# Optimization experiments

Hardware: AMD Instinct MI355X
Metric: run time of the kernel (lower is better)

Reference implementation:

```python
import jax, jax.numpy as jnp
import numpy as np

B, C, H, W = 4, 64, 256, 256
DS = 4        # ClusterLocalAtt downscale
CS = 2        # FastClusterAtt cluster_stride
NH = 4        # FastClusterAtt num_heads
G = 4         # OrthoConvClustering groups
N_NOISE = 8   # number of -1 (noise) labels; even and divisible by B


def _maxpool(x, k):
    b, c, h, w = x.shape
    return x.reshape(b, c, h // k, k, w // k, k).max(axis=(3, 5))


def _normalize(x, eps=1e-12):
    n = jnp.linalg.norm(x, axis=-1, keepdims=True)
    return x / jnp.maximum(n, eps)


def _feat_sim(cf, nf):
    # cf: (B,k,HW), nf: (B,n,HW) -> (B,k) mean cosine similarity over noise rows
    return jnp.einsum('bkl,bnl->bkn', _normalize(cf), _normalize(nf)).mean(-1)


def setup_inputs():
    key = jax.random.key(0)
    ks = jax.random.split(key, 12)
    x = jax.random.normal(ks[0], (B, C, H, W), jnp.float32)
    noise_idx = jnp.arange(N_NOISE, dtype=jnp.int32)
    labels = jax.random.randint(ks[1], (B * C,), 0, 12, dtype=jnp.int32)
    labels = labels.at[noise_idx].set(-1)
    inv = 1.0 / np.sqrt(C // G)
    return {
        'x': x, 'labels': labels, 'noise_idx': noise_idx,
        'qkv_w1': jax.random.normal(ks[2], (3 * C,), jnp.float32) * 0.5,
        'qkv_b1': jax.random.normal(ks[3], (3 * C,), jnp.float32) * 0.1,
        'up_k': jax.random.normal(ks[4], (C, DS, DS), jnp.float32) * 0.25,
        'up_b': jax.random.normal(ks[5], (C,), jnp.float32) * 0.1,
        'clu_w': jax.random.normal(ks[6], (G, C // G, C // G), jnp.float32) * inv,
        'clu_b': jnp.zeros((C,), jnp.float32),
        'qkv_w2': jax.random.normal(ks[7], (3 * C,), jnp.float32) * 0.5,
        'bais_w': jax.random.normal(ks[8], (C, C), jnp.float32) * (inv * 0.5),
        'bais_b': jax.random.normal(ks[9], (C,), jnp.float32) * 0.1,
    }


def reference(x, labels, noise_idx, qkv_w1, qkv_b1, up_k, up_b,
              clu_w, clu_b, qkv_w2, bais_w, bais_b):
    idx3 = jnp.arange(3 * C) // 3  # grouped 1x1 conv (groups=C): out ch j reads in ch j//3
    # ================= ClusterLocalAtt =================
    x_down = _maxpool(x, DS)                        # (B,C,Hd,Wd)
    Hd, Wd = H // DS, W // DS
    hw = Hd * Wd
    qkv = x_down[:, idx3] * qkv_w1[None, :, None, None] + qkv_b1[None, :, None, None]
    qkv = qkv.reshape(3 * B * C, hw)                # torch: reshape(1, 3*B*C, hw)
    q, k, v = jnp.split(qkv, 3, axis=0)             # each (B*C, hw) - batch/ch mixed, faithful
    valid = labels != -1
    allowed = (labels[:, None] == labels[None, :]) & valid[:, None] & valid[None, :]
    scores = q @ k.T                                # (BC, BC)
    attn = jax.nn.softmax(jnp.where(allowed, scores, -1e30), axis=-1)
    att = jnp.where(valid[:, None], attn @ v, 0.0)  # noise rows stay zero
    out = att.reshape(B, C, Hd, Wd)
    # depthwise ConvTranspose2d(kernel=DS, stride=DS): each input px -> DSxDS block
    up = jnp.einsum('bchw,cpq->bchpwq', out, up_k).reshape(B, C, H, W)
    up = up + up_b[None, :, None, None]
    noise = x.reshape(B * C, H * W)[noise_idx].reshape(B, N_NOISE // B, H * W)
    sim = _feat_sim(up.reshape(B, C, H * W), noise)[:, :, None, None]  # (B,C,1,1)
    out_clu = x + (up + (1.0 - sim) * x)
    # ================= FastClusterAtt =================
    xf = out_clu.reshape(B, G, C // G, H * W)
    xc = jnp.einsum('goi,bgil->bgol', clu_w, xf).reshape(B, C, H * W) + clu_b[None, :, None]
    x_ds = _maxpool(xc.reshape(B, C, H, W), CS)     # (B,C,Hs,Ws)
    Hs, Ws = H // CS, W // CS
    Ls = Hs * Ws
    qkv2 = (x_ds[:, idx3] * qkv_w2[None, :, None, None]).reshape(B, 3, NH, C // NH, Ls)
    qh, kh, vh = qkv2[:, 0], qkv2[:, 1], qkv2[:, 2]  # (B,NH,hd,Ls)
    sc = (qh * kh).sum(axis=2, keepdims=True) / np.sqrt(C // NH)  # (B,NH,1,Ls)
    a = jax.nn.softmax(sc, axis=-1)
    oh = (a * vh).sum(axis=-1).reshape(B, C)        # (B,C) global pooled heads
    # bilinear upsample of a spatially-constant map is the same constant -> skip interp
    ov = jnp.einsum('oc,bc->bo', bais_w, oh) + bais_b
    out_full = jnp.broadcast_to(ov[:, :, None, None], (B, C, H, W))
    sim2 = _feat_sim(out_full.reshape(B, C, H * W), noise)[:, :, None, None]
    WWT = jnp.einsum('goi,gpi->gop', clu_w, clu_w)
    I = jnp.eye(C // G, dtype=clu_w.dtype)
    ortho = 1.0 - jax.lax.stop_gradient(jnp.mean((WWT - I) ** 2))
    out2 = out_full * (1.0 - sim2) + ortho * out_clu
    return out_clu + out2
```

## Files before the change

kernel.cpp:

```cpp
#include <hip/hip_runtime.h>
#include <math.h>

#define WS_XD     0u
#define WS_S      1048576u
#define WS_GPART  1048832u
#define WS_G      2097408u
#define WS_COEF   2113792u
#define WS_CONST  2138368u
#define WS_ATT    2138624u
#define WS_FAC    3187200u
#define WS_XDS    3187456u
#define WS_OH     7381760u
#define WS_ALPHA  7382016u
#define WS_BETA   7382272u
#define WS_NSTAT  7382273u
#define WS_P2     7382304u

__device__ __forceinline__ float bsum(float v, float* sd, int tid) {
    sd[tid] = v; __syncthreads();
    for (int off = 128; off > 0; off >>= 1) {
        if (tid < off) sd[tid] += sd[tid + off];
        __syncthreads();
    }
    float r = sd[0]; __syncthreads(); return r;
}
__device__ __forceinline__ float bmax(float v, float* sd, int tid) {
    sd[tid] = v; __syncthreads();
    for (int off = 128; off > 0; off >>= 1) {
        if (tid < off) sd[tid] = fmaxf(sd[tid], sd[tid + off]);
        __syncthreads();
    }
    float r = sd[0]; __syncthreads(); return r;
}

__global__ __launch_bounds__(256) void k_noise(const float* __restrict__ x,
                                               const int* __restrict__ nidx,
                                               float* __restrict__ ws) {
    __shared__ float sd[256];
    int n = blockIdx.x, tid = threadIdx.x;
    const float4* xr = (const float4*)x + (size_t)nidx[n] * 16384;
    float s = 0.f, ss = 0.f;
    for (int it = 0; it < 64; ++it) {
        float4 v = xr[it * 256 + tid];
        s  += v.x + v.y + v.z + v.w;
        ss += v.x*v.x + v.y*v.y + v.z*v.z + v.w*v.w;
    }
    float st = bsum(s, sd, tid);
    float sst = bsum(ss, sd, tid);
    if (tid == 0) { ws[WS_NSTAT + n] = st; ws[WS_NSTAT + 8 + n] = sqrtf(sst); }
}

__global__ __launch_bounds__(256) void k_pool4(const float* __restrict__ x,
                                               float* __restrict__ ws) {
    __shared__ float sd[256];
    int r = blockIdx.x, tid = threadIdx.x;
    const float4* xr = (const float4*)x + (size_t)r * 16384;
    float* xd = ws + WS_XD + (size_t)r * 4096;
    float sum = 0.f;
    for (int it = 0; it < 16; ++it) {
        int o = it * 256 + tid;
        int h = o >> 6, w = o & 63;
        float m = -INFINITY;
        #pragma unroll
        for (int p = 0; p < 4; ++p) {
            float4 v = xr[(4 * h + p) * 64 + w];
            m = fmaxf(m, fmaxf(fmaxf(v.x, v.y), fmaxf(v.z, v.w)));
        }
        xd[o] = m; sum += m;
    }
    float st = bsum(sum, sd, tid);
    if (tid == 0) ws[WS_S + r] = st;
}

__global__ __launch_bounds__(256) void k_gram(float* __restrict__ ws) {
    __shared__ __align__(16) float As[64][68];
    __shared__ __align__(16) float Bs[64][68];
    int tid = threadIdx.x, tx = tid & 15, ty = tid >> 4;
    int ra0 = blockIdx.y * 64, rb0 = 80 + blockIdx.x * 64, k0 = blockIdx.z * 64;
    const float4* xd4 = (const float4*)(ws + WS_XD);
    #pragma unroll
    for (int q = 0; q < 4; ++q) {
        int idx = q * 256 + tid;
        int row = idx >> 4, cf = idx & 15;
        float4 a = xd4[(size_t)(ra0 + row) * 1024 + (k0 >> 2) + cf];
        As[cf*4+0][row] = a.x; As[cf*4+1][row] = a.y; As[cf*4+2][row] = a.z; As[cf*4+3][row] = a.w;
        float4 b = xd4[(size_t)(rb0 + row) * 1024 + (k0 >> 2) + cf];
        Bs[cf*4+0][row] = b.x; Bs[cf*4+1][row] = b.y; Bs[cf*4+2][row] = b.z; Bs[cf*4+3][row] = b.w;
    }
    __syncthreads();
    float acc[4][4] = {};
    #pragma unroll 4
    for (int kk = 0; kk < 64; ++kk) {
        float4 a = *(const float4*)&As[kk][ty * 4];
        float4 b = *(const float4*)&Bs[kk][tx * 4];
        acc[0][0] += a.x*b.x; acc[0][1] += a.x*b.y; acc[0][2] += a.x*b.z; acc[0][3] += a.x*b.w;
        acc[1][0] += a.y*b.x; acc[1][1] += a.y*b.y; acc[1][2] += a.y*b.z; acc[1][3] += a.y*b.w;
        acc[2][0] += a.z*b.x; acc[2][1] += a.z*b.y; acc[2][2] += a.z*b.z; acc[2][3] += a.z*b.w;
        acc[3][0] += a.w*b.x; acc[3][1] += a.w*b.y; acc[3][2] += a.w*b.z; acc[3][3] += a.w*b.w;
    }
    float* gp = ws + WS_GPART + (size_t)blockIdx.z * 16384;
    #pragma unroll
    for (int i = 0; i < 4; ++i) {
        float4 o = make_float4(acc[i][0], acc[i][1], acc[i][2], acc[i][3]);
        *(float4*)&gp[(size_t)(ra0 + ty * 4 + i) * 128 + blockIdx.x * 64 + tx * 4] = o;
    }
}

__global__ __launch_bounds__(256) void k_gred(float* __restrict__ ws) {
    int t = blockIdx.x * 256 + threadIdx.x;
    const float4* gp = (const float4*)(ws + WS_GPART);
    float4 s = make_float4(0.f, 0.f, 0.f, 0.f);
    for (int p = 0; p < 64; ++p) {
        float4 v = gp[(size_t)p * 4096 + t];
        s.x += v.x; s.y += v.y; s.z += v.z; s.w += v.w;
    }
    ((float4*)(ws + WS_G))[t] = s;
}

__global__ __launch_bounds__(256) void k_attn1(const int* __restrict__ labels,
                                               const float* __restrict__ w1,
                                               const float* __restrict__ b1,
                                               float* __restrict__ ws) {
    __shared__ float sd[256];
    __shared__ float attn_s[256];
    int i = blockIdx.x, tid = threadIdx.x;
    int labi = labels[i];
    bool validi = (labi != -1);
    int bi = (i >= 192) ? 1 : 0;
    int ji = i - bi * 192;
    int rq = bi * 64 + ji / 3;
    float wq = w1[ji], bq = b1[ji];
    int gk = 256 + tid;
    int bk = (gk >= 384) ? 2 : 1;
    int jk = gk - bk * 192;
    int rk = bk * 64 + jk / 3;
    float wk = w1[jk], bbk = b1[jk];
    int labj = labels[tid];
    bool allowed = validi && (labj == labi) && (labj != -1);
    float score = wq * wk * ws[WS_G + rq * 128 + (rk - 80)]
                + wq * bbk * ws[WS_S + rq]
                + wk * bq  * ws[WS_S + rk]
                + 4096.0f * bq * bbk;
    float sc = allowed ? score : -1e30f;
    float m = bmax(sc, sd, tid);
    float e = __expf(sc - m);
    float Z = bsum(e, sd, tid);
    float attn = validi ? (e / Z) : 0.0f;
    attn_s[tid] = attn;
    int gv = 512 + tid;
    int bv = (gv >= 576) ? 3 : 2;
    int jv = gv - bv * 192;
    float csum = bsum(attn * b1[jv], sd, tid);
    if (tid < 96) {
        float s = 0.0f;
        if (tid < 86) {
            int rv = 170 + tid;
            int lo, hi, jadd;
            if (rv < 192) { int c = rv - 128; lo = 3 * c; if (lo < 128) lo = 128; hi = 3 * c + 2; jadd = -128; }
            else          { int c = rv - 192; lo = 3 * c; hi = 3 * c + 2; jadd = 64; }
            for (int jj = lo; jj <= hi; ++jj) s += attn_s[jj + jadd] * w1[jj];
        }
        ws[WS_COEF + i * 96 + tid] = s;
    }
    if (tid == 0) ws[WS_CONST + i] = csum;
}

__global__ __launch_bounds__(256) void k_attmm(float* __restrict__ ws) {
    __shared__ __align__(16) float As[96][68];
    __shared__ __align__(16) float Bs[96][64];
    int tid = threadIdx.x, tx = tid & 15, ty = tid >> 4;
    int col0 = blockIdx.x * 64, row0 = blockIdx.y * 64;
    const float4* cf4 = (const float4*)(ws + WS_COEF);
    const float4* xd4 = (const float4*)(ws + WS_XD);
    #pragma unroll
    for (int q = 0; q < 6; ++q) {
        int f = q * 256 + tid;
        {
            int row = f / 24, c24 = f - row * 24;
            float4 v = cf4[(size_t)(row0 + row) * 24 + c24];
            As[c24*4+0][row] = v.x; As[c24*4+1][row] = v.y; As[c24*4+2][row] = v.z; As[c24*4+3][row] = v.w;
        }
        {
            int row = f >> 4, c16 = f & 15;
            float4 v = make_float4(0.f, 0.f, 0.f, 0.f);
            if (row < 86) v = xd4[(size_t)(170 + row) * 1024 + (col0 >> 2) + c16];
            *(float4*)&Bs[row][c16 * 4] = v;
        }
    }
    __syncthreads();
    float acc[4][4] = {};
    #pragma unroll 4
    for (int kk = 0; kk < 96; ++kk) {
        float4 a = *(const float4*)&As[kk][ty * 4];
        float4 b = *(const float4*)&Bs[kk][tx * 4];
        acc[0][0] += a.x*b.x; acc[0][1] += a.x*b.y; acc[0][2] += a.x*b.z; acc[0][3] += a.x*b.w;
        acc[1][0] += a.y*b.x; acc[1][1] += a.y*b.y; acc[1][2] += a.y*b.z; acc[1][3] += a.y*b.w;
        acc[2][0] += a.z*b.x; acc[2][1] += a.z*b.y; acc[2][2] += a.z*b.z; acc[2][3] += a.z*b.w;
        acc[3][0] += a.w*b.x; acc[3][1] += a.w*b.y; acc[3][2] += a.w*b.z; acc[3][3] += a.w*b.w;
    }
    float* att = ws + WS_ATT;
    #pragma unroll
    for (int i = 0; i < 4; ++i) {
        int row = row0 + ty * 4 + i;
        float cv = ws[WS_CONST + row];
        float4 o = make_float4(acc[i][0] + cv, acc[i][1] + cv, acc[i][2] + cv, acc[i][3] + cv);
        *(float4*)&att[(size_t)row * 4096 + col0 + tx * 4] = o;
    }
}

__global__ __launch_bounds__(256) void k_sim(const float* __restrict__ x,
                                             const int* __restrict__ nidx,
                                             const float* __restrict__ upk,
                                             const float* __restrict__ upb,
                                             float* __restrict__ ws) {
    __shared__ float sd[256];
    int r = blockIdx.x, tid = threadIdx.x;
    int b = r >> 6, c = r & 63;
    const float* att = ws + WS_ATT + (size_t)r * 4096;
    const float4* xn0 = (const float4*)x + (size_t)nidx[2 * b] * 16384;
    const float4* xn1 = (const float4*)x + (size_t)nidx[2 * b + 1] * 16384;
    const float4* k4p = (const float4*)upk + c * 4;
    float ub = upb[c];
    float4 kk0 = k4p[0], kk1 = k4p[1], kk2 = k4p[2], kk3 = k4p[3];
    float s2 = 0.f, d0 = 0.f, d1 = 0.f;
    for (int it = 0; it < 64; ++it) {
        int f = it * 256 + tid;
        int rowf = f >> 6, c4 = f & 63;
        float av = att[(rowf >> 2) * 64 + c4];
        int p = rowf & 3;
        float4 kv = (p == 0) ? kk0 : ((p == 1) ? kk1 : ((p == 2) ? kk2 : kk3));
        float4 a0 = xn0[f], a1 = xn1[f];
        float u;
        u = av * kv.x + ub; s2 += u * u; d0 += u * a0.x; d1 += u * a1.x;
        u = av * kv.y + ub; s2 += u * u; d0 += u * a0.y; d1 += u * a1.y;
        u = av * kv.z + ub; s2 += u * u; d0 += u * a0.z; d1 += u * a1.z;
        u = av * kv.w + ub; s2 += u * u; d0 += u * a0.w; d1 += u * a1.w;
    }
    s2 = bsum(s2, sd, tid);
    d0 = bsum(d0, sd, tid);
    d1 = bsum(d1, sd, tid);
    if (tid == 0) {
        float nup = fmaxf(sqrtf(s2), 1e-12f);
        float n0 = fmaxf(ws[WS_NSTAT + 8 + 2 * b], 1e-12f);
        float n1 = fmaxf(ws[WS_NSTAT + 8 + 2 * b + 1], 1e-12f);
        float sim = 0.5f * (d0 / (nup * n0) + d1 / (nup * n1));
        ws[WS_FAC + r] = 2.0f - sim;
    }
}

__global__ __launch_bounds__(256) void k_cluds(const float* __restrict__ x,
                                               const float* __restrict__ upk,
                                               const float* __restrict__ upb,
                                               const float* __restrict__ cw,
                                               const float* __restrict__ cb,
                                               float* __restrict__ ws) {
    __shared__ float wcl[256];
    __shared__ float kup[256];
    __shared__ float cbl[16], ubl[16], fcl[16];
    int h2 = blockIdx.x, g = blockIdx.y, b = blockIdx.z;
    int t = threadIdx.x;
    wcl[t] = cw[g * 256 + t];
    kup[t] = upk[g * 256 + t];
    if (t < 16) {
        cbl[t] = cb[g * 16 + t];
        ubl[t] = upb[g * 16 + t];
        fcl[t] = ws[WS_FAC + b * 64 + g * 16 + t];
    }
    __syncthreads();
    int r0 = 2 * h2;
    int h_att = h2 >> 1, p0 = r0 & 3;
    int wa = t >> 2, q = t & 3;
    float oc0[16], oc1[16];
    const float* attb = ws + WS_ATT;
    #pragma unroll
    for (int i = 0; i < 16; ++i) {
        int cch = g * 16 + i;
        float av = attb[(size_t)(b * 64 + cch) * 4096 + h_att * 64 + wa];
        float u0 = av * kup[i * 16 + p0 * 4 + q] + ubl[i];
        float u1 = av * kup[i * 16 + (p0 + 1) * 4 + q] + ubl[i];
        const float* xrow = x + (size_t)(b * 64 + cch) * 65536;
        float x0 = xrow[r0 * 256 + t];
        float x1 = xrow[(r0 + 1) * 256 + t];
        oc0[i] = u0 + fcl[i] * x0;
        oc1[i] = u1 + fcl[i] * x1;
    }
    float* xds = ws + WS_XDS;
    #pragma unroll
    for (int o = 0; o < 16; ++o) {
        float a0 = cbl[o], a1 = cbl[o];
        #pragma unroll
        for (int i = 0; i < 16; ++i) {
            a0 += wcl[o * 16 + i] * oc0[i];
            a1 += wcl[o * 16 + i] * oc1[i];
        }
        float m = fmaxf(a0, a1);
        m = fmaxf(m, __shfl_xor(m, 1));
        if ((t & 1) == 0)
            xds[(size_t)((b * 64 + g * 16 + o) * 128 + h2) * 128 + (t >> 1)] = m;
    }
}

__global__ __launch_bounds__(256) void k_attn2a(const float* __restrict__ w2,
                                                float* __restrict__ ws) {
    __shared__ float ms[256], dsh[256];
    __shared__ float ns[256][16];
    int chunk = blockIdx.x, nh = blockIdx.y, b = blockIdx.z, tid = threadIdx.x;
    const float* X = ws + WS_XDS + (size_t)b * 1048576;
    float wqd[16], wkd[16], wvd[16];
    int oq[16], ok[16], ovo[16];
    #pragma unroll
    for (int d = 0; d < 16; ++d) {
        int jq = nh * 16 + d, jk = 64 + nh * 16 + d, jv = 128 + nh * 16 + d;
        wqd[d] = w2[jq]; wkd[d] = w2[jk]; wvd[d] = w2[jv];
        oq[d] = (jq / 3) * 16384; ok[d] = (jk / 3) * 16384; ovo[d] = (jv / 3) * 16384;
    }
    float m = -INFINITY, den = 0.f, num[16];
    #pragma unroll
    for (int d = 0; d < 16; ++d) num[d] = 0.f;
    #pragma unroll
    for (int e = 0; e < 2; ++e) {
        int l = chunk * 512 + e * 256 + tid;
        float sc = 0.f;
        #pragma unroll
        for (int d = 0; d < 16; ++d) sc += (X[oq[d] + l] * wqd[d]) * (X[ok[d] + l] * wkd[d]);
        sc *= 0.25f;
        float nm = fmaxf(m, sc);
        float rr = __expf(m - nm), ee = __expf(sc - nm);
        den = den * rr + ee;
        #pragma unroll
        for (int d = 0; d < 16; ++d) num[d] = num[d] * rr + ee * (X[ovo[d] + l] * wvd[d]);
        m = nm;
    }
    ms[tid] = m; dsh[tid] = den;
    #pragma unroll
    for (int d = 0; d < 16; ++d) ns[tid][d] = num[d];
    __syncthreads();
    for (int off = 128; off > 0; off >>= 1) {
        if (tid < off) {
            float ma = ms[tid], mb = ms[tid + off];
            float M = fmaxf(ma, mb);
            float ra = __expf(ma - M), rb = __expf(mb - M);
            dsh[tid] = dsh[tid] * ra + dsh[tid + off] * rb;
            #pragma unroll
            for (int d = 0; d < 16; ++d)
                ns[tid][d] = ns[tid][d] * ra + ns[tid + off][d] * rb;
            ms[tid] = M;
        }
        __syncthreads();
    }
    if (tid == 0) {
        float* p = ws + WS_P2 + ((size_t)(b * 4 + nh) * 32 + chunk) * 18;
        p[0] = ms[0]; p[1] = dsh[0];
        #pragma unroll
        for (int d = 0; d < 16; ++d) p[2 + d] = ns[0][d];
    }
}

__global__ __launch_bounds__(64) void k_attn2b(float* __restrict__ ws) {
    int bh = blockIdx.x;
    int lane = threadIdx.x;
    float m = -INFINITY, den = 0.f, num[16];
    #pragma unroll
    for (int d = 0; d < 16; ++d) num[d] = 0.f;
    if (lane < 32) {
        const float* p = ws + WS_P2 + ((size_t)bh * 32 + lane) * 18;
        m = p[0]; den = p[1];
        #pragma unroll
        for (int d = 0; d < 16; ++d) num[d] = p[2 + d];
    }
    #pragma unroll
    for (int mask = 1; mask <= 16; mask <<= 1) {
        float mo = __shfl_xor(m, mask);
        float dn = __shfl_xor(den, mask);
        float M = fmaxf(m, mo);
        float ra = __expf(m - M), rb = __expf(mo - M);
        den = den * ra + dn * rb;
        #pragma unroll
        for (int d = 0; d < 16; ++d) {
            float no = __shfl_xor(num[d], mask);
            num[d] = num[d] * ra + no * rb;
        }
        m = M;
    }
    __shared__ float outn[16];
    __shared__ float outd;
    if (lane == 0) {
        outd = den;
        #pragma unroll
        for (int d = 0; d < 16; ++d) outn[d] = num[d];
    }
    __syncthreads();
    if (lane < 16) {
        int b = bh >> 2, nh = bh & 3;
        ws[WS_OH + b * 64 + nh * 16 + lane] = outn[lane] / outd;
    }
}

__global__ __launch_bounds__(256) void k_head(const float* __restrict__ bw,
                                              const float* __restrict__ bb,
                                              const float* __restrict__ cw,
                                              float* __restrict__ ws) {
    __shared__ float ohs[256], sd[256];
    int tid = threadIdx.x;
    ohs[tid] = ws[WS_OH + tid];
    __syncthreads();
    int b = tid >> 6, o = tid & 63;
    float s = bb[o];
    #pragma unroll 4
    for (int c2 = 0; c2 < 64; ++c2) s += bw[o * 64 + c2] * ohs[b * 64 + c2];
    float oacc = 0.f;
    for (int u = 0; u < 4; ++u) {
        int e = tid * 4 + u;
        int g = e >> 8, oo = (e >> 4) & 15, p = e & 15;
        float ss = 0.f;
        #pragma unroll
        for (int i = 0; i < 16; ++i) ss += cw[g * 256 + oo * 16 + i] * cw[g * 256 + p * 16 + i];
        float dd = ss - ((oo == p) ? 1.0f : 0.0f);
        oacc += dd * dd;
    }
    float tot = bsum(oacc, sd, tid);
    float nd = fmaxf(fabsf(s) * 256.0f, 1e-12f);
    float t0 = ws[WS_NSTAT + 2 * b], t1 = ws[WS_NSTAT + 2 * b + 1];
    float n0 = fmaxf(ws[WS_NSTAT + 8 + 2 * b], 1e-12f);
    float n1 = fmaxf(ws[WS_NSTAT + 8 + 2 * b + 1], 1e-12f);
    float sim2 = (s / nd) * 0.5f * (t0 / n0 + t1 / n1);
    ws[WS_ALPHA + tid] = (1.0f - sim2) * s;
    if (tid == 0) ws[WS_BETA] = 2.0f - tot / 1024.0f;
}

__global__ __launch_bounds__(256) void k_final(const float* __restrict__ x,
                                               const float* __restrict__ upk,
                                               const float* __restrict__ upb,
                                               const float* __restrict__ ws,
                                               float* __restrict__ out) {
    int idx = blockIdx.x * 256 + threadIdx.x;
    int r = idx >> 14;
    int rem = idx & 16383;
    int rowf = rem >> 6, c4 = rem & 63;
    int c = r & 63;
    float av = ws[WS_ATT + (size_t)r * 4096 + (rowf >> 2) * 64 + c4];
    int p = rowf & 3;
    float4 kv = ((const float4*)upk)[c * 4 + p];
    float ub = upb[c];
    float fac = ws[WS_FAC + r], al = ws[WS_ALPHA + r], be = ws[WS_BETA];
    float4 xv = ((const float4*)x)[idx];
    float4 o;
    o.x = be * (av * kv.x + ub + fac * xv.x) + al;
    o.y = be * (av * kv.y + ub + fac * xv.y) + al;
    o.z = be * (av * kv.z + ub + fac * xv.z) + al;
    o.w = be * (av * kv.w + ub + fac * xv.w) + al;
    ((float4*)out)[idx] = o;
}

extern "C" void kernel_launch(void* const* d_in, const int* in_sizes, int n_in,
                              void* d_out, int out_size, void* d_ws, size_t ws_size,
                              hipStream_t stream) {
    const float* x      = (const float*)d_in[0];
    const int*   labels = (const int*)d_in[1];
    const int*   nidx   = (const int*)d_in[2];
    const float* w1     = (const float*)d_in[3];
    const float* b1     = (const float*)d_in[4];
    const float* upk    = (const float*)d_in[5];
    const float* upb    = (const float*)d_in[6];
    const float* cw     = (const float*)d_in[7];
    const float* cb     = (const float*)d_in[8];
    const float* w2     = (const float*)d_in[9];
    const float* bw     = (const float*)d_in[10];
    const float* bb     = (const float*)d_in[11];
    float* ws  = (float*)d_ws;
    float* out = (float*)d_out;

    hipLaunchKernelGGL(k_noise,  dim3(8),          dim3(256), 0, stream, x, nidx, ws);
    hipLaunchKernelGGL(k_pool4,  dim3(256),        dim3(256), 0, stream, x, ws);
    hipLaunchKernelGGL(k_gram,   dim3(2, 2, 64),   dim3(256), 0, stream, ws);
    hipLaunchKernelGGL(k_gred,   dim3(16),         dim3(256), 0, stream, ws);
    hipLaunchKernelGGL(k_attn1,  dim3(256),        dim3(256), 0, stream, labels, w1, b1, ws);
    hipLaunchKernelGGL(k_attmm,  dim3(64, 4),      dim3(256), 0, stream, ws);
    hipLaunchKernelGGL(k_sim,    dim3(256),        dim3(256), 0, stream, x, nidx, upk, upb, ws);
    hipLaunchKernelGGL(k_cluds,  dim3(128, 4, 4),  dim3(256), 0, stream, x, upk, upb, cw, cb, ws);
    hipLaunchKernelGGL(k_attn2a, dim3(32, 4, 4),   dim3(256), 0, stream, w2, ws);
    hipLaunchKernelGGL(k_attn2b, dim3(16),         dim3(64),  0, stream, ws);
    hipLaunchKernelGGL(k_head,   dim3(1),          dim3(256), 0, stream, bw, bb, cw, ws);
    hipLaunchKernelGGL(k_final,  dim3(16384),      dim3(256), 0, stream, x, upk, upb, ws, out);
}
```

Baseline: 119.8 us.

## Fuse cluster conv, downsample and attention softmax into one kernel

Folds the noise-row statistics into the 4x4 max-pool pass so x is not read a second time for those rows. Merges the cluster 1x1 conv, 2x2 max-pool and second attention into one kernel that keeps the downsampled features in registers, so the intermediate XDS buffer is no longer written and read back. The attention partial reduction and the head kernel are merged into a single tail kernel. The trade-off is fewer launches and less global traffic against a 64-float register array per thread, which can cut occupancy, and only 256 blocks in the fused kernel.

```diff
diff --git a/kernel.cpp b/kernel.cpp
--- a/kernel.cpp
+++ b/kernel.cpp
@@ -9,8 +9,6 @@
 #define WS_CONST  2138368u
 #define WS_ATT    2138624u
 #define WS_FAC    3187200u
-#define WS_XDS    3187456u
-#define WS_OH     7381760u
 #define WS_ALPHA  7382016u
 #define WS_BETA   7382272u
 #define WS_NSTAT  7382273u
@@ -33,30 +31,14 @@
     float r = sd[0]; __syncthreads(); return r;
 }
 
-__global__ __launch_bounds__(256) void k_noise(const float* __restrict__ x,
+__global__ __launch_bounds__(256) void k_pool4(const float* __restrict__ x,
                                                const int* __restrict__ nidx,
-                                               float* __restrict__ ws) {
-    __shared__ float sd[256];
-    int n = blockIdx.x, tid = threadIdx.x;
-    const float4* xr = (const float4*)x + (size_t)nidx[n] * 16384;
-    float s = 0.f, ss = 0.f;
-    for (int it = 0; it < 64; ++it) {
-        float4 v = xr[it * 256 + tid];
-        s  += v.x + v.y + v.z + v.w;
-        ss += v.x*v.x + v.y*v.y + v.z*v.z + v.w*v.w;
-    }
-    float st = bsum(s, sd, tid);
-    float sst = bsum(ss, sd, tid);
-    if (tid == 0) { ws[WS_NSTAT + n] = st; ws[WS_NSTAT + 8 + n] = sqrtf(sst); }
-}
-
-__global__ __launch_bounds__(256) void k_pool4(const float* __restrict__ x,
                                                float* __restrict__ ws) {
     __shared__ float sd[256];
     int r = blockIdx.x, tid = threadIdx.x;
     const float4* xr = (const float4*)x + (size_t)r * 16384;
     float* xd = ws + WS_XD + (size_t)r * 4096;
-    float sum = 0.f;
+    float sum = 0.f, s = 0.f, ss = 0.f;
     for (int it = 0; it < 16; ++it) {
         int o = it * 256 + tid;
         int h = o >> 6, w = o & 63;
@@ -65,11 +47,24 @@
         for (int p = 0; p < 4; ++p) {
             float4 v = xr[(4 * h + p) * 64 + w];
             m = fmaxf(m, fmaxf(fmaxf(v.x, v.y), fmaxf(v.z, v.w)));
+            s  += v.x + v.y + v.z + v.w;
+            ss += v.x*v.x + v.y*v.y + v.z*v.z + v.w*v.w;
         }
         xd[o] = m; sum += m;
     }
     float st = bsum(sum, sd, tid);
     if (tid == 0) ws[WS_S + r] = st;
+    bool isn = false;
+    #pragma unroll
+    for (int n = 0; n < 8; ++n) isn = isn || (nidx[n] == r);
+    if (isn) {
+        float ts = bsum(s, sd, tid);
+        float tss = bsum(ss, sd, tid);
+        if (tid == 0) {
+            for (int n = 0; n < 8; ++n)
+                if (nidx[n] == r) { ws[WS_NSTAT + n] = ts; ws[WS_NSTAT + 8 + n] = sqrtf(tss); }
+        }
+    }
 }
 
 __global__ __launch_bounds__(256) void k_gram(float* __restrict__ ws) {
@@ -248,161 +243,169 @@
     }
 }
 
-__global__ __launch_bounds__(256) void k_cluds(const float* __restrict__ x,
+__global__ __launch_bounds__(256) void k_cluat(const float* __restrict__ x,
                                                const float* __restrict__ upk,
                                                const float* __restrict__ upb,
                                                const float* __restrict__ cw,
                                                const float* __restrict__ cb,
+                                               const float* __restrict__ w2,
                                                float* __restrict__ ws) {
-    __shared__ float wcl[256];
-    __shared__ float kup[256];
-    __shared__ float cbl[16], ubl[16], fcl[16];
-    int h2 = blockIdx.x, g = blockIdx.y, b = blockIdx.z;
-    int t = threadIdx.x;
-    wcl[t] = cw[g * 256 + t];
-    kup[t] = upk[g * 256 + t];
-    if (t < 16) {
-        cbl[t] = cb[g * 16 + t];
-        ubl[t] = upb[g * 16 + t];
-        fcl[t] = ws[WS_FAC + b * 64 + g * 16 + t];
-    }
+    __shared__ float wcl[1024];
+    __shared__ float kup[1024];
+    __shared__ float cbl[64], ubl[64], fcl[64];
+    __shared__ float wl2[192];
+    __shared__ float red[4][4][18];
+    int hp = blockIdx.x, b = blockIdx.y, t = threadIdx.x;
+    #pragma unroll
+    for (int q = 0; q < 4; ++q) {
+        wcl[q * 256 + t] = cw[q * 256 + t];
+        kup[q * 256 + t] = upk[q * 256 + t];
+    }
+    if (t < 64) {
+        cbl[t] = cb[t];
+        ubl[t] = upb[t];
+        fcl[t] = ws[WS_FAC + b * 64 + t];
+    }
+    if (t < 192) wl2[t] = w2[t];
     __syncthreads();
+
+    int h2 = hp * 2 + (t >> 7);
+    int w = t & 127;
     int r0 = 2 * h2;
-    int h_att = h2 >> 1, p0 = r0 & 3;
-    int wa = t >> 2, q = t & 3;
-    float oc0[16], oc1[16];
+    int p0 = r0 & 3;
+    int q0 = (2 * w) & 3;
+    int h_att = hp;
+    int wa = w >> 1;
+
     const float* attb = ws + WS_ATT;
-    #pragma unroll
-    for (int i = 0; i < 16; ++i) {
-        int cch = g * 16 + i;
-        float av = attb[(size_t)(b * 64 + cch) * 4096 + h_att * 64 + wa];
-        float u0 = av * kup[i * 16 + p0 * 4 + q] + ubl[i];
-        float u1 = av * kup[i * 16 + (p0 + 1) * 4 + q] + ubl[i];
-        const float* xrow = x + (size_t)(b * 64 + cch) * 65536;
-        float x0 = xrow[r0 * 256 + t];
-        float x1 = xrow[(r0 + 1) * 256 + t];
-        oc0[i] = u0 + fcl[i] * x0;
-        oc1[i] = u1 + fcl[i] * x1;
-    }
-    float* xds = ws + WS_XDS;
-    #pragma unroll
-    for (int o = 0; o < 16; ++o) {
-        float a0 = cbl[o], a1 = cbl[o];
+    float xv[64];
+    #pragma unroll
+    for (int g = 0; g < 4; ++g) {
+        float oc[16][4];
         #pragma unroll
         for (int i = 0; i < 16; ++i) {
-            a0 += wcl[o * 16 + i] * oc0[i];
-            a1 += wcl[o * 16 + i] * oc1[i];
-        }
-        float m = fmaxf(a0, a1);
-        m = fmaxf(m, __shfl_xor(m, 1));
-        if ((t & 1) == 0)
-            xds[(size_t)((b * 64 + g * 16 + o) * 128 + h2) * 128 + (t >> 1)] = m;
-    }
-}
-
-__global__ __launch_bounds__(256) void k_attn2a(const float* __restrict__ w2,
-                                                float* __restrict__ ws) {
-    __shared__ float ms[256], dsh[256];
-    __shared__ float ns[256][16];
-    int chunk = blockIdx.x, nh = blockIdx.y, b = blockIdx.z, tid = threadIdx.x;
-    const float* X = ws + WS_XDS + (size_t)b * 1048576;
-    float wqd[16], wkd[16], wvd[16];
-    int oq[16], ok[16], ovo[16];
-    #pragma unroll
-    for (int d = 0; d < 16; ++d) {
-        int jq = nh * 16 + d, jk = 64 + nh * 16 + d, jv = 128 + nh * 16 + d;
-        wqd[d] = w2[jq]; wkd[d] = w2[jk]; wvd[d] = w2[jv];
-        oq[d] = (jq / 3) * 16384; ok[d] = (jk / 3) * 16384; ovo[d] = (jv / 3) * 16384;
-    }
-    float m = -INFINITY, den = 0.f, num[16];
-    #pragma unroll
-    for (int d = 0; d < 16; ++d) num[d] = 0.f;
-    #pragma unroll
-    for (int e = 0; e < 2; ++e) {
-        int l = chunk * 512 + e * 256 + tid;
+            int ch = g * 16 + i;
+            float av = attb[(size_t)(b * 64 + ch) * 4096 + h_att * 64 + wa];
+            const float* xc = x + (size_t)(b * 64 + ch) * 65536;
+            float2 x0 = *(const float2*)&xc[r0 * 256 + 2 * w];
+            float2 x1 = *(const float2*)&xc[(r0 + 1) * 256 + 2 * w];
+            float ub = ubl[ch], fc = fcl[ch];
+            oc[i][0] = av * kup[ch * 16 + p0 * 4 + q0]       + ub + fc * x0.x;
+            oc[i][1] = av * kup[ch * 16 + p0 * 4 + q0 + 1]   + ub + fc * x0.y;
+            oc[i][2] = av * kup[ch * 16 + (p0 + 1) * 4 + q0]     + ub + fc * x1.x;
+            oc[i][3] = av * kup[ch * 16 + (p0 + 1) * 4 + q0 + 1] + ub + fc * x1.y;
+        }
+        #pragma unroll
+        for (int o = 0; o < 16; ++o) {
+            float cbv = cbl[g * 16 + o];
+            float a0 = cbv, a1 = cbv, a2 = cbv, a3 = cbv;
+            #pragma unroll
+            for (int i = 0; i < 16; ++i) {
+                float wv = wcl[(g * 16 + o) * 16 + i];
+                a0 += wv * oc[i][0]; a1 += wv * oc[i][1];
+                a2 += wv * oc[i][2]; a3 += wv * oc[i][3];
+            }
+            xv[g * 16 + o] = fmaxf(fmaxf(a0, a1), fmaxf(a2, a3));
+        }
+    }
+
+    int wave = t >> 6, lane = t & 63;
+    #pragma unroll
+    for (int nh = 0; nh < 4; ++nh) {
         float sc = 0.f;
         #pragma unroll
-        for (int d = 0; d < 16; ++d) sc += (X[oq[d] + l] * wqd[d]) * (X[ok[d] + l] * wkd[d]);
+        for (int d = 0; d < 16; ++d) {
+            int jq = nh * 16 + d, jk = 64 + nh * 16 + d;
+            sc += (xv[jq / 3] * wl2[jq]) * (xv[jk / 3] * wl2[jk]);
+        }
         sc *= 0.25f;
-        float nm = fmaxf(m, sc);
-        float rr = __expf(m - nm), ee = __expf(sc - nm);
-        den = den * rr + ee;
-        #pragma unroll
-        for (int d = 0; d < 16; ++d) num[d] = num[d] * rr + ee * (X[ovo[d] + l] * wvd[d]);
-        m = nm;
-    }
-    ms[tid] = m; dsh[tid] = den;
-    #pragma unroll
-    for (int d = 0; d < 16; ++d) ns[tid][d] = num[d];
-    __syncthreads();
-    for (int off = 128; off > 0; off >>= 1) {
-        if (tid < off) {
-            float ma = ms[tid], mb = ms[tid + off];
-            float M = fmaxf(ma, mb);
-            float ra = __expf(ma - M), rb = __expf(mb - M);
-            dsh[tid] = dsh[tid] * ra + dsh[tid + off] * rb;
+        float num[16];
+        #pragma unroll
+        for (int d = 0; d < 16; ++d) {
+            int jv = 128 + nh * 16 + d;
+            num[d] = xv[jv / 3] * wl2[jv];
+        }
+        float m = sc, den = 1.f;
+        #pragma unroll
+        for (int mask = 1; mask <= 32; mask <<= 1) {
+            float mo = __shfl_xor(m, mask);
+            float dn = __shfl_xor(den, mask);
+            float M = fmaxf(m, mo);
+            float ra = __expf(m - M), rb = __expf(mo - M);
+            den = den * ra + dn * rb;
             #pragma unroll
             for (int d = 0; d < 16; ++d)
-                ns[tid][d] = ns[tid][d] * ra + ns[tid + off][d] * rb;
-            ms[tid] = M;
-        }
-        __syncthreads();
-    }
-    if (tid == 0) {
-        float* p = ws + WS_P2 + ((size_t)(b * 4 + nh) * 32 + chunk) * 18;
-        p[0] = ms[0]; p[1] = dsh[0];
-        #pragma unroll
-        for (int d = 0; d < 16; ++d) p[2 + d] = ns[0][d];
-    }
-}
-
-__global__ __launch_bounds__(64) void k_attn2b(float* __restrict__ ws) {
-    int bh = blockIdx.x;
-    int lane = threadIdx.x;
+                num[d] = num[d] * ra + __shfl_xor(num[d], mask) * rb;
+            m = M;
+        }
+        if (lane == 0) {
+            red[wave][nh][0] = m; red[wave][nh][1] = den;
+            #pragma unroll
+            for (int d = 0; d < 16; ++d) red[wave][nh][2 + d] = num[d];
+        }
+    }
+    __syncthreads();
+    if (t < 4) {
+        float m = -INFINITY, den = 0.f, num[16];
+        #pragma unroll
+        for (int d = 0; d < 16; ++d) num[d] = 0.f;
+        #pragma unroll
+        for (int wv = 0; wv < 4; ++wv) {
+            float mo = red[wv][t][0], dn = red[wv][t][1];
+            float M = fmaxf(m, mo);
+            float ra = __expf(m - M), rb = __expf(mo - M);
+            den = den * ra + dn * rb;
+            #pragma unroll
+            for (int d = 0; d < 16; ++d)
+                num[d] = num[d] * ra + red[wv][t][2 + d] * rb;
+            m = M;
+        }
+        float* p = ws + WS_P2 + ((size_t)(b * 4 + t) * 64 + hp) * 18;
+        p[0] = m; p[1] = den;
+        #pragma unroll
+        for (int d = 0; d < 16; ++d) p[2 + d] = num[d];
+    }
+}
+
+__global__ __launch_bounds__(256) void k_tail(const float* __restrict__ bw,
+                                              const float* __restrict__ bb,
+                                              const float* __restrict__ cw,
+                                              float* __restrict__ ws) {
+    __shared__ float ohs[256], sd[256];
+    int tid = threadIdx.x;
+    int grp = tid >> 4;
+    int j = tid & 15;
     float m = -INFINITY, den = 0.f, num[16];
     #pragma unroll
     for (int d = 0; d < 16; ++d) num[d] = 0.f;
-    if (lane < 32) {
-        const float* p = ws + WS_P2 + ((size_t)bh * 32 + lane) * 18;
-        m = p[0]; den = p[1];
-        #pragma unroll
-        for (int d = 0; d < 16; ++d) num[d] = p[2 + d];
-    }
-    #pragma unroll
-    for (int mask = 1; mask <= 16; mask <<= 1) {
+    #pragma unroll
+    for (int u = 0; u < 4; ++u) {
+        const float* p = ws + WS_P2 + ((size_t)grp * 64 + j * 4 + u) * 18;
+        float mo = p[0], dn = p[1];
+        float M = fmaxf(m, mo);
+        float ra = __expf(m - M), rb = __expf(mo - M);
+        den = den * ra + dn * rb;
+        #pragma unroll
+        for (int d = 0; d < 16; ++d) num[d] = num[d] * ra + p[2 + d] * rb;
+        m = M;
+    }
+    #pragma unroll
+    for (int mask = 1; mask <= 8; mask <<= 1) {
         float mo = __shfl_xor(m, mask);
         float dn = __shfl_xor(den, mask);
         float M = fmaxf(m, mo);
         float ra = __expf(m - M), rb = __expf(mo - M);
         den = den * ra + dn * rb;
         #pragma unroll
-        for (int d = 0; d < 16; ++d) {
-            float no = __shfl_xor(num[d], mask);
-            num[d] = num[d] * ra + no * rb;
-        }
+        for (int d = 0; d < 16; ++d)
+            num[d] = num[d] * ra + __shfl_xor(num[d], mask) * rb;
         m = M;
     }
-    __shared__ float outn[16];
-    __shared__ float outd;
-    if (lane == 0) {
-        outd = den;
-        #pragma unroll
-        for (int d = 0; d < 16; ++d) outn[d] = num[d];
-    }
-    __syncthreads();
-    if (lane < 16) {
-        int b = bh >> 2, nh = bh & 3;
-        ws[WS_OH + b * 64 + nh * 16 + lane] = outn[lane] / outd;
-    }
-}
-
-__global__ __launch_bounds__(256) void k_head(const float* __restrict__ bw,
-                                              const float* __restrict__ bb,
-                                              const float* __restrict__ cw,
-                                              float* __restrict__ ws) {
-    __shared__ float ohs[256], sd[256];
-    int tid = threadIdx.x;
-    ohs[tid] = ws[WS_OH + tid];
+    if (j == 0) {
+        int b = grp >> 2, nh = grp & 3;
+        #pragma unroll
+        for (int d = 0; d < 16; ++d) ohs[b * 64 + nh * 16 + d] = num[d] / den;
+    }
     __syncthreads();
     int b = tid >> 6, o = tid & 63;
     float s = bb[o];
@@ -470,16 +473,13 @@
     float* ws  = (float*)d_ws;
     float* out = (float*)d_out;
 
-    hipLaunchKernelGGL(k_noise,  dim3(8),          dim3(256), 0, stream, x, nidx, ws);
-    hipLaunchKernelGGL(k_pool4,  dim3(256),        dim3(256), 0, stream, x, ws);
+    hipLaunchKernelGGL(k_pool4,  dim3(256),        dim3(256), 0, stream, x, nidx, ws);
     hipLaunchKernelGGL(k_gram,   dim3(2, 2, 64),   dim3(256), 0, stream, ws);
     hipLaunchKernelGGL(k_gred,   dim3(16),         dim3(256), 0, stream, ws);
     hipLaunchKernelGGL(k_attn1,  dim3(256),        dim3(256), 0, stream, labels, w1, b1, ws);
     hipLaunchKernelGGL(k_attmm,  dim3(64, 4),      dim3(256), 0, stream, ws);
     hipLaunchKernelGGL(k_sim,    dim3(256),        dim3(256), 0, stream, x, nidx, upk, upb, ws);
-    hipLaunchKernelGGL(k_cluds,  dim3(128, 4, 4),  dim3(256), 0, stream, x, upk, upb, cw, cb, ws);
-    hipLaunchKernelGGL(k_attn2a, dim3(32, 4, 4),   dim3(256), 0, stream, w2, ws);
-    hipLaunchKernelGGL(k_attn2b, dim3(16),         dim3(64),  0, stream, ws);
-    hipLaunchKernelGGL(k_head,   dim3(1),          dim3(256), 0, stream, bw, bb, cw, ws);
+    hipLaunchKernelGGL(k_cluat,  dim3(64, 4),      dim3(256), 0, stream, x, upk, upb, cw, cb, w2, ws);
+    hipLaunchKernelGGL(k_tail,   dim3(1),          dim3(256), 0, stream, bw, bb, cw, ws);
     hipLaunchKernelGGL(k_final,  dim3(16384),      dim3(256), 0, stream, x, upk, upb, ws, out);
 }
```

Measured after the change: 217.1 us. +81.2%, slower.
